# Kernel tuning notes

Measured on AMD Instinct MI355X. Metric: run time of the kernel, lower is better.

## Reference

```python
import jax, jax.numpy as jnp
import numpy as np

B, SRC_LEN, IN_DIM = 4096, 128, 16
H = 64
SEQ_LEN = 100
MEAN_DIM = 4
COV_DIM = MEAN_DIM + MEAN_DIM * (MEAN_DIM - 1) // 2  # 10
SKIP = 4


def _lin_init(key, out_d, in_d):
    k1, k2 = jax.random.split(key)
    bound = 1.0 / np.sqrt(in_d)
    W = jax.random.uniform(k1, (out_d, in_d), minval=-bound, maxval=bound, dtype=jnp.float32)
    b = jax.random.uniform(k2, (out_d,), minval=-bound, maxval=bound, dtype=jnp.float32)
    return W, b


def setup_inputs() -> dict:
    key = jax.random.key(0)
    ks = jax.random.split(key, 16)
    inp = {}
    inp["x"] = jax.random.normal(ks[0], (B, SRC_LEN, IN_DIM), dtype=jnp.float32)
    inp["trg"] = jax.random.normal(ks[1], (B, 1, SKIP), dtype=jnp.float32)
    # encoder GRU (1 layer)
    inp["enc_Wih"], inp["enc_bih"] = _lin_init(ks[2], 3 * H, IN_DIM)
    inp["enc_Whh"], inp["enc_bhh"] = _lin_init(ks[3], 3 * H, H)
    # decoder GRU (1 layer)
    inp["dec_Wih"], inp["dec_bih"] = _lin_init(ks[4], 3 * H, IN_DIM)
    inp["dec_Whh"], inp["dec_bhh"] = _lin_init(ks[5], 3 * H, H)
    # decoder.out: Linear(H -> IN_DIM)
    inp["out_W"], inp["out_b"] = _lin_init(ks[6], IN_DIM, H)
    # initEmbed: Linear(SKIP -> IN_DIM)
    inp["emb_W"], inp["emb_b"] = _lin_init(ks[7], IN_DIM, SKIP)
    # mean head: Linear(IN_DIM->H), GELU, Linear(H->MEAN_DIM)
    inp["mh_W1"], inp["mh_b1"] = _lin_init(ks[8], H, IN_DIM)
    inp["mh_W2"], inp["mh_b2"] = _lin_init(ks[9], MEAN_DIM, H)
    # cov head: Linear(IN_DIM->H), GELU, Linear(H->COV_DIM)
    inp["ch_W1"], inp["ch_b1"] = _lin_init(ks[10], H, IN_DIM)
    inp["ch_W2"], inp["ch_b2"] = _lin_init(ks[11], COV_DIM, H)
    return inp


def _gru_cell(h, xt, Wih, Whh, bih, bhh):
    # PyTorch GRU cell math. h, xt: [B, H], [B, in]
    gi = xt @ Wih.T + bih           # [B, 3H]
    gh = h @ Whh.T + bhh            # [B, 3H]
    i_r, i_z, i_n = jnp.split(gi, 3, axis=-1)
    h_r, h_z, h_n = jnp.split(gh, 3, axis=-1)
    r = jax.nn.sigmoid(i_r + h_r)
    z = jax.nn.sigmoid(i_z + h_z)
    n = jnp.tanh(i_n + r * h_n)
    return (1.0 - z) * n + z * h


def reference(x, trg, enc_Wih, enc_bih, enc_Whh, enc_bhh,
              dec_Wih, dec_bih, dec_Whh, dec_bhh,
              out_W, out_b, emb_W, emb_b,
              mh_W1, mh_b1, mh_W2, mh_b2,
              ch_W1, ch_b1, ch_W2, ch_b2):
    b = x.shape[0]
    # ---- encoder GRU over src_len; only final hidden is used downstream ----
    h0 = jnp.zeros((b, H), dtype=x.dtype)

    def enc_step(h, xt):
        h = _gru_cell(h, xt, enc_Wih, enc_Whh, enc_bih, enc_bhh)
        return h, None

    enc_h, _ = jax.lax.scan(enc_step, h0, jnp.swapaxes(x, 0, 1))

    init_in = trg[:, 0, :] @ emb_W.T + emb_b  # [B, IN_DIM]

    def dec_step(carry, _):
        h, inp = carry
        h = _gru_cell(h, inp, dec_Wih, dec_Whh, dec_bih, dec_bhh)
        o = h @ out_W.T + out_b               # [B, IN_DIM]
        nxt = jax.lax.stop_gradient(o)        # .detach() on fed-back input
        return (h, nxt), o

    (_, _), outs = jax.lax.scan(dec_step, (enc_h, init_in), None, length=SEQ_LEN)
    dec_out = jnp.swapaxes(outs, 0, 1)        # [B, SEQ_LEN, IN_DIM]

    # ---- output heads (Dropout is identity in eval) ----
    means = jax.nn.gelu(dec_out @ mh_W1.T + mh_b1, approximate=False) @ mh_W2.T + mh_b2
    covs = jax.nn.gelu(dec_out @ ch_W1.T + ch_b1, approximate=False) @ ch_W2.T + ch_b2

    inf = jnp.inf
    lower = jnp.array([-inf, -inf, -1.0, -1.0], dtype=means.dtype)
    upper = jnp.array([inf, inf, 1.0, 1.0], dtype=means.dtype)
    means = jnp.maximum(jnp.minimum(means, upper), lower)
    return means, covs
```

## Files before the change

### kernel.cpp

```cpp
#include <hip/hip_runtime.h>
#include <cstdint>
#include <cstddef>

#define BTOT    4096
#define SRCLEN  128
#define INDIM   16
#define HDIM    64
#define SEQLEN  100
#define MEANS_N (BTOT * SEQLEN * 4)

__device__ __forceinline__ float sigmoidf_(float x) {
    return __builtin_amdgcn_rcpf(1.0f + __expf(-x));
}
__device__ __forceinline__ float tanhf_(float x) {
    float e = __expf(2.0f * x);
    return 1.0f - 2.0f * __builtin_amdgcn_rcpf(e + 1.0f);
}
__device__ __forceinline__ float gelu_fast(float x) {
    float z = fabsf(x) * 0.70710678118654752440f;
    float t = __builtin_amdgcn_rcpf(1.0f + 0.3275911f * z);
    float p = t * (0.254829592f +
              t * (-0.284496736f +
              t * (1.421413741f +
              t * (-1.453152027f +
              t * 1.061405429f))));
    float er = 1.0f - p * __expf(-z * z);
    er = copysignf(er, x);
    return 0.5f * x * (1.0f + er);
}

typedef __attribute__((ext_vector_type(8))) short s8v;
typedef __attribute__((ext_vector_type(4))) float f4v;

__device__ __forceinline__ unsigned short f2bf(float x) {
    unsigned u = __float_as_uint(x);
    unsigned r = (u + 0x7FFFu + ((u >> 16) & 1u)) >> 16;
    return (unsigned short)r;
}
__device__ __forceinline__ float bf2f(unsigned short b) {
    return __uint_as_float(((unsigned)b) << 16);
}
__device__ __forceinline__ void split2(float4 a, float4 b, s8v& hi, s8v& lo) {
    float v[8] = {a.x, a.y, a.z, a.w, b.x, b.y, b.z, b.w};
    #pragma unroll
    for (int j = 0; j < 8; ++j) {
        unsigned short h = f2bf(v[j]);
        hi[j] = (short)h;
        lo[j] = (short)f2bf(v[j] - bf2f(h));
    }
}
__device__ __forceinline__ void split8(const float* v, s8v& hi, s8v& lo) {
    #pragma unroll
    for (int j = 0; j < 8; ++j) {
        unsigned short h = f2bf(v[j]);
        hi[j] = (short)h;
        lo[j] = (short)f2bf(v[j] - bf2f(h));
    }
}
__device__ __forceinline__ void load_bfrag(const float* p, s8v& hi, s8v& lo) {
    float4 a = *(const float4*)p;
    float4 b = *(const float4*)(p + 4);
    split2(a, b, hi, lo);
}

__device__ __forceinline__ float half_merge(float own_lo, float send_hi, int lane) {
    float rec = __shfl_xor(send_hi, 32, 64);
    return (lane < 32) ? own_lo : rec;
}

#define MFMA16(a, b, c) __builtin_amdgcn_mfma_f32_16x16x32_bf16((a), (b), (c), 0, 0, 0)

__global__ __launch_bounds__(256, 2) void enc_mfma_kernel(
    const float* __restrict__ x,
    const float* __restrict__ Wih, const float* __restrict__ bih,
    const float* __restrict__ Whh, const float* __restrict__ bhh,
    float* __restrict__ enc_h)
{
    const int tid  = threadIdx.x;
    const int lane = tid & 63;
    const int w    = tid >> 6;
    const int col  = lane & 15;
    const int q    = lane >> 4;
    const int u    = w * 16 + col;
    const int b0   = blockIdx.x * 8;
    const int rj0  = (q & 1) * 4 + ((q >> 1) << 1);

    __shared__ __align__(16) unsigned short hiL[2][16][72];
    __shared__ __align__(16) unsigned short loL[2][16][72];
    __shared__ __align__(16) unsigned short xhi_l[64][8][16];
    __shared__ __align__(16) unsigned short xlo_l[64][8][16];

    for (int i = tid; i < 2 * 16 * 72; i += 256) {
        ((unsigned short*)hiL)[i] = 0;
        ((unsigned short*)loL)[i] = 0;
    }

    auto stage_x = [&](int c) {
        #pragma unroll
        for (int k = 0; k < 8; ++k) {
            int f   = tid + k * 256;
            int b   = f >> 8;
            int rem = f & 255;
            int tl  = rem >> 2;
            int d4  = (rem & 3) << 2;
            const float* xp = x + ((size_t)(b0 + b) * SRCLEN + (c * 64 + tl)) * INDIM + d4;
            float4 v = *(const float4*)xp;
            float vv[4] = {v.x, v.y, v.z, v.w};
            unsigned short hh[4], ll[4];
            #pragma unroll
            for (int j = 0; j < 4; ++j) {
                hh[j] = f2bf(vv[j]);
                ll[j] = f2bf(vv[j] - bf2f(hh[j]));
            }
            *(ushort4*)&xhi_l[tl][b][d4] = make_ushort4(hh[0], hh[1], hh[2], hh[3]);
            *(ushort4*)&xlo_l[tl][b][d4] = make_ushort4(ll[0], ll[1], ll[2], ll[3]);
        }
    };

    const s8v z8 = {0, 0, 0, 0, 0, 0, 0, 0};
    const f4v z4 = {0.0f, 0.0f, 0.0f, 0.0f};

    s8v brh[3], brl[3], bzh[3], bzl[3], bnhh[2], bnhl[2], bnxh, bnxl;
    load_bfrag(Whh + (size_t)u * 64 + q * 8,              brh[0], brl[0]);
    load_bfrag(Whh + (size_t)u * 64 + 32 + q * 8,         brh[1], brl[1]);
    load_bfrag(Whh + (size_t)(64 + u) * 64 + q * 8,       bzh[0], bzl[0]);
    load_bfrag(Whh + (size_t)(64 + u) * 64 + 32 + q * 8,  bzh[1], bzl[1]);
    load_bfrag(Whh + (size_t)(128 + u) * 64 + q * 8,      bnhh[0], bnhl[0]);
    load_bfrag(Whh + (size_t)(128 + u) * 64 + 32 + q * 8, bnhh[1], bnhl[1]);
    if (q < 2) {
        load_bfrag(Wih + (size_t)u * 16 + q * 8,         brh[2], brl[2]);
        load_bfrag(Wih + (size_t)(64 + u) * 16 + q * 8,  bzh[2], bzl[2]);
        load_bfrag(Wih + (size_t)(128 + u) * 16 + q * 8, bnxh, bnxl);
    } else {
        brh[2] = z8; brl[2] = z8; bzh[2] = z8; bzl[2] = z8; bnxh = z8; bnxl = z8;
    }

    const float br   = bih[u] + bhh[u];
    const float bz   = bih[u + 64] + bhh[u + 64];
    const float bnx  = bih[u + 128];
    const float bnh  = bhh[u + 128];

    stage_x(0);
    float hold2[2] = {0.0f, 0.0f};
    __syncthreads();

    int cur = 0;
    for (int t = 0; t < SRCLEN; ++t) {
        if (t == 64) {
            stage_x(1);
            __syncthreads();
        }
        const int tl = t & 63;

        s8v xh, xl;
        if (q < 2 && col < 8) {
            xh = *(const s8v*)&xhi_l[tl][col][q * 8];
            xl = *(const s8v*)&xlo_l[tl][col][q * 8];
        } else { xh = z8; xl = z8; }

        const s8v ah0 = *(const s8v*)&hiL[cur][col][q * 8];
        const s8v al0 = *(const s8v*)&loL[cur][col][q * 8];
        const s8v ah1 = *(const s8v*)&hiL[cur][col][32 + q * 8];
        const s8v al1 = *(const s8v*)&loL[cur][col][32 + q * 8];

        f4v accr, accz, accnh, accnx;
        accr  = MFMA16(ah0, brh[0], z4);
        accz  = MFMA16(ah0, bzh[0], z4);
        accnh = MFMA16(ah0, bnhh[0], z4);
        accr  = MFMA16(ah0, brl[0], accr);
        accz  = MFMA16(ah0, bzl[0], accz);
        accnh = MFMA16(ah0, bnhl[0], accnh);
        accr  = MFMA16(al0, brh[0], accr);
        accz  = MFMA16(al0, bzh[0], accz);
        accnh = MFMA16(al0, bnhh[0], accnh);
        accr  = MFMA16(ah1, brh[1], accr);
        accz  = MFMA16(ah1, bzh[1], accz);
        accnh = MFMA16(ah1, bnhh[1], accnh);
        accr  = MFMA16(ah1, brl[1], accr);
        accz  = MFMA16(ah1, bzl[1], accz);
        accnh = MFMA16(ah1, bnhl[1], accnh);
        accr  = MFMA16(al1, brh[1], accr);
        accz  = MFMA16(al1, bzh[1], accz);
        accnh = MFMA16(al1, bnhh[1], accnh);
        accr  = MFMA16(xh, brh[2], accr);
        accz  = MFMA16(xh, bzh[2], accz);
        accnx = MFMA16(xh, bnxh, z4);
        accr  = MFMA16(xh, brl[2], accr);
        accz  = MFMA16(xh, bzl[2], accz);
        accnx = MFMA16(xh, bnxl, accnx);
        accr  = MFMA16(xl, brh[2], accr);
        accz  = MFMA16(xl, bzh[2], accz);
        accnx = MFMA16(xl, bnxh, accnx);

        float pr[2], pz[2], pnh[2], pnx[2];
        pr[0]  = half_merge(accr[0],  accr[2],  lane);
        pr[1]  = half_merge(accr[1],  accr[3],  lane);
        pz[0]  = half_merge(accz[0],  accz[2],  lane);
        pz[1]  = half_merge(accz[1],  accz[3],  lane);
        pnh[0] = half_merge(accnh[0], accnh[2], lane);
        pnh[1] = half_merge(accnh[1], accnh[3], lane);
        pnx[0] = half_merge(accnx[0], accnx[2], lane);
        pnx[1] = half_merge(accnx[1], accnx[3], lane);

        const int nxt = cur ^ 1;
        #pragma unroll
        for (int j = 0; j < 2; ++j) {
            float r  = sigmoidf_(pr[j] + br);
            float zz = sigmoidf_(pz[j] + bz);
            float n  = tanhf_(pnx[j] + bnx + r * (pnh[j] + bnh));
            float h  = (1.0f - zz) * n + zz * hold2[j];
            hold2[j] = h;
            unsigned short hh = f2bf(h);
            hiL[nxt][rj0 + j][u] = hh;
            loL[nxt][rj0 + j][u] = f2bf(h - bf2f(hh));
        }
        __syncthreads();
        cur ^= 1;
    }

    enc_h[(size_t)(b0 + rj0) * HDIM + u]     = hold2[0];
    enc_h[(size_t)(b0 + rj0 + 1) * HDIM + u] = hold2[1];
}

__global__ __launch_bounds__(256, 2) void dec_mfma_kernel(
    const float* __restrict__ trg,
    const float* __restrict__ Wih, const float* __restrict__ bih,
    const float* __restrict__ Whh, const float* __restrict__ bhh,
    const float* __restrict__ outW, const float* __restrict__ outb,
    const float* __restrict__ embW, const float* __restrict__ embb,
    const float* __restrict__ enc_h,
    float* __restrict__ dec_o)
{
    const int tid  = threadIdx.x;
    const int lane = tid & 63;
    const int w    = tid >> 6;
    const int col  = lane & 15;
    const int q    = lane >> 4;
    const int u    = w * 16 + col;
    const int b0   = blockIdx.x * 8;
    const int rj0  = (q & 1) * 4 + ((q >> 1) << 1);

    __shared__ __align__(16) unsigned short hiL[2][16][72];
    __shared__ __align__(16) unsigned short loL[2][16][72];
    __shared__ float outW_l[16][64];
    __shared__ float init_l[8][16];

    for (int i = tid; i < 16 * 64; i += 256) outW_l[i >> 6][i & 63] = outW[i];
    if (tid < 128) {
        int b = tid >> 4, jj = tid & 15;
        float s = embb[jj];
        #pragma unroll
        for (int s4 = 0; s4 < 4; ++s4)
            s = fmaf(embW[jj * 4 + s4], trg[(size_t)(b0 + b) * 4 + s4], s);
        init_l[b][jj] = s;
    }
    for (int i = tid; i < 2 * 8 * 72; i += 256) {
        int buf = i / (8 * 72);
        int rr  = (i / 72) & 7;
        int cc  = i % 72;
        hiL[buf][8 + rr][cc] = 0;
        loL[buf][8 + rr][cc] = 0;
    }
    if (tid < 128) {
        int idx = tid * 4;
        int bb = idx >> 6, uu = idx & 63;
        float4 v = *(const float4*)(enc_h + (size_t)(b0 + bb) * HDIM + uu);
        float vv[4] = {v.x, v.y, v.z, v.w};
        #pragma unroll
        for (int j = 0; j < 4; ++j) {
            unsigned short hh = f2bf(vv[j]);
            hiL[0][bb][uu + j] = hh;
            loL[0][bb][uu + j] = f2bf(vv[j] - bf2f(hh));
        }
    }
    float hold2[2];
    hold2[0] = enc_h[(size_t)(b0 + rj0) * HDIM + u];
    hold2[1] = enc_h[(size_t)(b0 + rj0 + 1) * HDIM + u];

    __syncthreads();

    const f4v z4 = {0.0f, 0.0f, 0.0f, 0.0f};

    float wh_r[16], wh_z[16], wh_n[16];
    #pragma unroll
    for (int c = 0; c < 2; ++c)
        #pragma unroll
        for (int jj = 0; jj < 8; ++jj) {
            int k = c * 32 + q * 8 + jj;
            wh_r[c * 8 + jj] = Whh[(size_t)u * 64 + k];
            wh_z[c * 8 + jj] = Whh[(size_t)(64 + u) * 64 + k];
            wh_n[c * 8 + jj] = Whh[(size_t)(128 + u) * 64 + k];
        }
    float wi_r[16], wi_z[16], wi_n[16];
    #pragma unroll
    for (int j = 0; j < 16; ++j) {
        wi_r[j] = Wih[(size_t)u * 16 + j];
        wi_z[j] = Wih[(size_t)(64 + u) * 16 + j];
        wi_n[j] = Wih[(size_t)(128 + u) * 16 + j];
    }

    float m_r[16], m_z[16], c_in[16];
    #pragma unroll
    for (int c = 0; c < 2; ++c)
        #pragma unroll
        for (int jj = 0; jj < 8; ++jj) {
            int k = c * 32 + q * 8 + jj;
            float sr = 0.0f, sz = 0.0f, sn = 0.0f;
            #pragma unroll
            for (int j = 0; j < 16; ++j) {
                float ow = outW_l[j][k];
                sr = fmaf(wi_r[j], ow, sr);
                sz = fmaf(wi_z[j], ow, sz);
                sn = fmaf(wi_n[j], ow, sn);
            }
            m_r[c * 8 + jj]  = wh_r[c * 8 + jj] + sr;
            m_z[c * 8 + jj]  = wh_z[c * 8 + jj] + sz;
            c_in[c * 8 + jj] = sn;
        }

    s8v mrh[2], mrl[2], mzh[2], mzl[2], cinh[2], cinl[2], hnh[2], hnl[2];
    split8(m_r,      mrh[0],  mrl[0]);  split8(m_r + 8,  mrh[1],  mrl[1]);
    split8(m_z,      mzh[0],  mzl[0]);  split8(m_z + 8,  mzh[1],  mzl[1]);
    split8(c_in,     cinh[0], cinl[0]); split8(c_in + 8, cinh[1], cinl[1]);
    split8(wh_n,     hnh[0],  hnl[0]);  split8(wh_n + 8, hnh[1],  hnl[1]);
    s8v r0h[2], r0l[2], z0h[2], z0l[2];
    split8(wh_r, r0h[0], r0l[0]); split8(wh_r + 8, r0h[1], r0l[1]);
    split8(wh_z, z0h[0], z0l[0]); split8(wh_z + 8, z0h[1], z0l[1]);
    s8v owh[2], owl[2];
    {
        float ov[16];
        #pragma unroll
        for (int c = 0; c < 2; ++c)
            #pragma unroll
            for (int jj = 0; jj < 8; ++jj)
                ov[c * 8 + jj] = outW_l[col][c * 32 + q * 8 + jj];
        split8(ov, owh[0], owl[0]); split8(ov + 8, owh[1], owl[1]);
    }

    float b_r = bhh[u] + bih[u];
    float b_z = bhh[u + 64] + bih[u + 64];
    float b_in = bih[u + 128];
    const float b_hn = bhh[u + 128];
    #pragma unroll
    for (int j = 0; j < 16; ++j) {
        float obj = outb[j];
        b_r  = fmaf(obj, wi_r[j], b_r);
        b_z  = fmaf(obj, wi_z[j], b_z);
        b_in = fmaf(obj, wi_n[j], b_in);
    }
    const float ob = outb[col];

    float g_r[2], g_z[2], g_n[2];
    #pragma unroll
    for (int j2 = 0; j2 < 2; ++j2) {
        int row = rj0 + j2;
        float sr = bih[u] + bhh[u];
        float sz = bih[u + 64] + bhh[u + 64];
        float sn = bih[u + 128];
        #pragma unroll
        for (int j = 0; j < 16; ++j) {
            float iv = init_l[row][j];
            sr = fmaf(wi_r[j], iv, sr);
            sz = fmaf(wi_z[j], iv, sz);
            sn = fmaf(wi_n[j], iv, sn);
        }
        g_r[j2] = sr; g_z[j2] = sz; g_n[j2] = sn;
    }

    {
        const s8v ah0 = *(const s8v*)&hiL[0][col][q * 8];
        const s8v al0 = *(const s8v*)&loL[0][col][q * 8];
        const s8v ah1 = *(const s8v*)&hiL[0][col][32 + q * 8];
        const s8v al1 = *(const s8v*)&loL[0][col][32 + q * 8];
        f4v ar, az, ahn;
        ar  = MFMA16(ah0, r0h[0], z4);
        az  = MFMA16(ah0, z0h[0], z4);
        ahn = MFMA16(ah0, hnh[0], z4);
        ar  = MFMA16(ah0, r0l[0], ar);
        az  = MFMA16(ah0, z0l[0], az);
        ahn = MFMA16(ah0, hnl[0], ahn);
        ar  = MFMA16(al0, r0h[0], ar);
        az  = MFMA16(al0, z0h[0], az);
        ahn = MFMA16(al0, hnh[0], ahn);
        ar  = MFMA16(ah1, r0h[1], ar);
        az  = MFMA16(ah1, z0h[1], az);
        ahn = MFMA16(ah1, hnh[1], ahn);
        ar  = MFMA16(ah1, r0l[1], ar);
        az  = MFMA16(ah1, z0l[1], az);
        ahn = MFMA16(ah1, hnl[1], ahn);
        ar  = MFMA16(al1, r0h[1], ar);
        az  = MFMA16(al1, z0h[1], az);
        ahn = MFMA16(al1, hnh[1], ahn);

        float pr[2], pz[2], pnh[2];
        pr[0]  = half_merge(ar[0],  ar[2],  lane);
        pr[1]  = half_merge(ar[1],  ar[3],  lane);
        pz[0]  = half_merge(az[0],  az[2],  lane);
        pz[1]  = half_merge(az[1],  az[3],  lane);
        pnh[0] = half_merge(ahn[0], ahn[2], lane);
        pnh[1] = half_merge(ahn[1], ahn[3], lane);

        #pragma unroll
        for (int j = 0; j < 2; ++j) {
            float r  = sigmoidf_(pr[j] + g_r[j]);
            float zz = sigmoidf_(pz[j] + g_z[j]);
            float n  = tanhf_(g_n[j] + r * (pnh[j] + b_hn));
            float h  = (1.0f - zz) * n + zz * hold2[j];
            hold2[j] = h;
            unsigned short hh = f2bf(h);
            hiL[1][rj0 + j][u] = hh;
            loL[1][rj0 + j][u] = f2bf(h - bf2f(hh));
        }
        __syncthreads();
    }

    for (int t = 1; t < SEQLEN; ++t) {
        const int cur = t & 1;
        const s8v ah0 = *(const s8v*)&hiL[cur][col][q * 8];
        const s8v al0 = *(const s8v*)&loL[cur][col][q * 8];
        const s8v ah1 = *(const s8v*)&hiL[cur][col][32 + q * 8];
        const s8v al1 = *(const s8v*)&loL[cur][col][32 + q * 8];

        if (w == 0) {
            f4v oa;
            oa = MFMA16(ah0, owh[0], z4);
            oa = MFMA16(ah0, owl[0], oa);
            oa = MFMA16(al0, owh[0], oa);
            oa = MFMA16(ah1, owh[1], oa);
            oa = MFMA16(ah1, owl[1], oa);
            oa = MFMA16(al1, owh[1], oa);
            if (q < 2) {
                #pragma unroll
                for (int i = 0; i < 4; ++i)
                    dec_o[(((size_t)(b0 + q * 4 + i) * SEQLEN) + (t - 1)) * INDIM + col] = oa[i] + ob;
            }
        }

        f4v ar, az, ain, ahn;
        ar  = MFMA16(ah0, mrh[0], z4);
        az  = MFMA16(ah0, mzh[0], z4);
        ain = MFMA16(ah0, cinh[0], z4);
        ahn = MFMA16(ah0, hnh[0], z4);
        ar  = MFMA16(ah0, mrl[0], ar);
        az  = MFMA16(ah0, mzl[0], az);
        ain = MFMA16(ah0, cinl[0], ain);
        ahn = MFMA16(ah0, hnl[0], ahn);
        ar  = MFMA16(al0, mrh[0], ar);
        az  = MFMA16(al0, mzh[0], az);
        ain = MFMA16(al0, cinh[0], ain);
        ahn = MFMA16(al0, hnh[0], ahn);
        ar  = MFMA16(ah1, mrh[1], ar);
        az  = MFMA16(ah1, mzh[1], az);
        ain = MFMA16(ah1, cinh[1], ain);
        ahn = MFMA16(ah1, hnh[1], ahn);
        ar  = MFMA16(ah1, mrl[1], ar);
        az  = MFMA16(ah1, mzl[1], az);
        ain = MFMA16(ah1, cinl[1], ain);
        ahn = MFMA16(ah1, hnl[1], ahn);
        ar  = MFMA16(al1, mrh[1], ar);
        az  = MFMA16(al1, mzh[1], az);
        ain = MFMA16(al1, cinh[1], ain);
        ahn = MFMA16(al1, hnh[1], ahn);

        float pr[2], pz[2], pin[2], pnh[2];
        pr[0]  = half_merge(ar[0],  ar[2],  lane);
        pr[1]  = half_merge(ar[1],  ar[3],  lane);
        pz[0]  = half_merge(az[0],  az[2],  lane);
        pz[1]  = half_merge(az[1],  az[3],  lane);
        pin[0] = half_merge(ain[0], ain[2], lane);
        pin[1] = half_merge(ain[1], ain[3], lane);
        pnh[0] = half_merge(ahn[0], ahn[2], lane);
        pnh[1] = half_merge(ahn[1], ahn[3], lane);

        const int nxt = cur ^ 1;
        #pragma unroll
        for (int j = 0; j < 2; ++j) {
            float r  = sigmoidf_(pr[j] + b_r);
            float zz = sigmoidf_(pz[j] + b_z);
            float n  = tanhf_(pin[j] + b_in + r * (pnh[j] + b_hn));
            float h  = (1.0f - zz) * n + zz * hold2[j];
            hold2[j] = h;
            unsigned short hh = f2bf(h);
            hiL[nxt][rj0 + j][u] = hh;
            loL[nxt][rj0 + j][u] = f2bf(h - bf2f(hh));
        }
        __syncthreads();
    }

    if (w == 0) {
        const s8v ah0 = *(const s8v*)&hiL[0][col][q * 8];
        const s8v al0 = *(const s8v*)&loL[0][col][q * 8];
        const s8v ah1 = *(const s8v*)&hiL[0][col][32 + q * 8];
        const s8v al1 = *(const s8v*)&loL[0][col][32 + q * 8];
        f4v oa;
        oa = MFMA16(ah0, owh[0], z4);
        oa = MFMA16(ah0, owl[0], oa);
        oa = MFMA16(al0, owh[0], oa);
        oa = MFMA16(ah1, owh[1], oa);
        oa = MFMA16(ah1, owl[1], oa);
        oa = MFMA16(al1, owh[1], oa);
        if (q < 2) {
            #pragma unroll
            for (int i = 0; i < 4; ++i)
                dec_o[(((size_t)(b0 + q * 4 + i) * SEQLEN) + (SEQLEN - 1)) * INDIM + col] = oa[i] + ob;
        }
    }
}

__global__ void heads_kernel(
    const float* __restrict__ dec_o,
    const float* __restrict__ mW1, const float* __restrict__ mb1,
    const float* __restrict__ mW2, const float* __restrict__ mb2,
    const float* __restrict__ cW1, const float* __restrict__ cb1,
    const float* __restrict__ cW2, const float* __restrict__ cb2,
    float* __restrict__ out)
{
    const size_t r = (size_t)blockIdx.x * 256 + threadIdx.x;

    float o16[16];
    {
        const float4* op = (const float4*)(dec_o + r * 16);
        #pragma unroll
        for (int c = 0; c < 4; ++c) {
            float4 v = op[c];
            o16[4 * c + 0] = v.x; o16[4 * c + 1] = v.y;
            o16[4 * c + 2] = v.z; o16[4 * c + 3] = v.w;
        }
    }

    float m[4], cv[10];
    #pragma unroll
    for (int j = 0; j < 4; ++j)  m[j]  = mb2[j];
    #pragma unroll
    for (int j = 0; j < 10; ++j) cv[j] = cb2[j];

    #pragma unroll 8
    for (int hu = 0; hu < 64; ++hu) {
        const float* w1m = mW1 + hu * 16;
        float hm = mb1[hu];
        #pragma unroll
        for (int i = 0; i < 16; ++i) hm = fmaf(w1m[i], o16[i], hm);
        float gm = gelu_fast(hm);
        #pragma unroll
        for (int j = 0; j < 4; ++j) m[j] = fmaf(mW2[j * 64 + hu], gm, m[j]);

        const float* w1c = cW1 + hu * 16;
        float hc = cb1[hu];
        #pragma unroll
        for (int i = 0; i < 16; ++i) hc = fmaf(w1c[i], o16[i], hc);
        float gc = gelu_fast(hc);
        #pragma unroll
        for (int j = 0; j < 10; ++j) cv[j] = fmaf(cW2[j * 64 + hu], gc, cv[j]);
    }

    m[2] = fminf(fmaxf(m[2], -1.0f), 1.0f);
    m[3] = fminf(fmaxf(m[3], -1.0f), 1.0f);

    float* means = out;
    float* covs  = out + MEANS_N;
    #pragma unroll
    for (int j = 0; j < 4; ++j)  means[r * 4 + j]  = m[j];
    #pragma unroll
    for (int j = 0; j < 10; ++j) covs[r * 10 + j]  = cv[j];
}

extern "C" void kernel_launch(void* const* d_in, const int* in_sizes, int n_in,
                              void* d_out, int out_size, void* d_ws, size_t ws_size,
                              hipStream_t stream)
{
    const float* x    = (const float*)d_in[0];
    const float* trg  = (const float*)d_in[1];
    const float* eWih = (const float*)d_in[2];
    const float* ebih = (const float*)d_in[3];
    const float* eWhh = (const float*)d_in[4];
    const float* ebhh = (const float*)d_in[5];
    const float* dWih = (const float*)d_in[6];
    const float* dbih = (const float*)d_in[7];
    const float* dWhh = (const float*)d_in[8];
    const float* dbhh = (const float*)d_in[9];
    const float* outW = (const float*)d_in[10];
    const float* outb = (const float*)d_in[11];
    const float* embW = (const float*)d_in[12];
    const float* embb = (const float*)d_in[13];
    const float* mW1  = (const float*)d_in[14];
    const float* mb1  = (const float*)d_in[15];
    const float* mW2  = (const float*)d_in[16];
    const float* mb2  = (const float*)d_in[17];
    const float* cW1  = (const float*)d_in[18];
    const float* cb1  = (const float*)d_in[19];
    const float* cW2  = (const float*)d_in[20];
    const float* cb2  = (const float*)d_in[21];

    float* ws    = (float*)d_ws;
    float* enc_h = ws;
    float* dec_o = ws + (size_t)BTOT * HDIM;
    float* outp  = (float*)d_out;

    enc_mfma_kernel<<<dim3(BTOT / 8), dim3(256), 0, stream>>>(x, eWih, ebih, eWhh, ebhh, enc_h);
    dec_mfma_kernel<<<dim3(BTOT / 8), dim3(256), 0, stream>>>(trg, dWih, dbih, dWhh, dbhh,
                                                              outW, outb, embW, embb, enc_h, dec_o);
    heads_kernel<<<dim3((BTOT * SEQLEN) / 256), dim3(256), 0, stream>>>(
        dec_o, mW1, mb1, mW2, mb2, cW1, cb1, cW2, cb2, outp);
}
```

Measured before the change: 388.3 us.

## Use permlane32_swap merges, branchless x loads, rotated output wave, LDS-staged head weights

Replaces the shfl_xor-based half merge with the permlane32_swap builtin, which avoids an LDS-routed shuffle on the critical recurrent path. Adds a zero-padded row to the staged x buffers so the per-step x fragment loads become unconditional. Rotates which wave computes the decoder output projection each step instead of always wave 0, spreading that load across waves. Stages the head weights into shared memory as float4-readable rows to replace scalar global loads. The permlane32_swap builtin depends on gfx950 support, and the extra LDS use raises shared-memory footprint.

```diff
diff --git a/kernel.cpp b/kernel.cpp
--- a/kernel.cpp
+++ b/kernel.cpp
@@ -63,9 +63,12 @@
     split2(a, b, hi, lo);
 }
 
-__device__ __forceinline__ float half_merge(float own_lo, float send_hi, int lane) {
-    float rec = __shfl_xor(send_hi, 32, 64);
-    return (lane < 32) ? own_lo : rec;
+typedef __attribute__((ext_vector_type(2))) unsigned int u2v;
+__device__ __forceinline__ float half_merge(float own_lo, float send_hi) {
+    u2v r = __builtin_amdgcn_permlane32_swap(__float_as_uint(own_lo),
+                                             __float_as_uint(send_hi),
+                                             false, false);
+    return __uint_as_float(r[0]);
 }
 
 #define MFMA16(a, b, c) __builtin_amdgcn_mfma_f32_16x16x32_bf16((a), (b), (c), 0, 0, 0)
@@ -87,12 +90,16 @@
 
     __shared__ __align__(16) unsigned short hiL[2][16][72];
     __shared__ __align__(16) unsigned short loL[2][16][72];
-    __shared__ __align__(16) unsigned short xhi_l[64][8][16];
-    __shared__ __align__(16) unsigned short xlo_l[64][8][16];
+    __shared__ __align__(16) unsigned short xhi_l[64][9][16];
+    __shared__ __align__(16) unsigned short xlo_l[64][9][16];
 
     for (int i = tid; i < 2 * 16 * 72; i += 256) {
         ((unsigned short*)hiL)[i] = 0;
         ((unsigned short*)loL)[i] = 0;
+    }
+    for (int i = tid; i < 64 * 16; i += 256) {
+        xhi_l[i >> 4][8][i & 15] = 0;
+        xlo_l[i >> 4][8][i & 15] = 0;
     }
 
     auto stage_x = [&](int c) {
@@ -140,6 +147,11 @@
     const float bnx  = bih[u + 128];
     const float bnh  = bhh[u + 128];
 
+    const int xb   = (q < 2) ? (col & 7) : 8;
+    const int xoff = (q & 1) * 8;
+    const unsigned short* xh_base = &xhi_l[0][xb][xoff];
+    const unsigned short* xl_base = &xlo_l[0][xb][xoff];
+
     stage_x(0);
     float hold2[2] = {0.0f, 0.0f};
     __syncthreads();
@@ -152,11 +164,8 @@
         }
         const int tl = t & 63;
 
-        s8v xh, xl;
-        if (q < 2 && col < 8) {
-            xh = *(const s8v*)&xhi_l[tl][col][q * 8];
-            xl = *(const s8v*)&xlo_l[tl][col][q * 8];
-        } else { xh = z8; xl = z8; }
+        const s8v xh = *(const s8v*)(xh_base + (size_t)tl * 144);
+        const s8v xl = *(const s8v*)(xl_base + (size_t)tl * 144);
 
         const s8v ah0 = *(const s8v*)&hiL[cur][col][q * 8];
         const s8v al0 = *(const s8v*)&loL[cur][col][q * 8];
@@ -193,14 +202,14 @@
         accnx = MFMA16(xl, bnxh, accnx);
 
         float pr[2], pz[2], pnh[2], pnx[2];
-        pr[0]  = half_merge(accr[0],  accr[2],  lane);
-        pr[1]  = half_merge(accr[1],  accr[3],  lane);
-        pz[0]  = half_merge(accz[0],  accz[2],  lane);
-        pz[1]  = half_merge(accz[1],  accz[3],  lane);
-        pnh[0] = half_merge(accnh[0], accnh[2], lane);
-        pnh[1] = half_merge(accnh[1], accnh[3], lane);
-        pnx[0] = half_merge(accnx[0], accnx[2], lane);
-        pnx[1] = half_merge(accnx[1], accnx[3], lane);
+        pr[0]  = half_merge(accr[0],  accr[2]);
+        pr[1]  = half_merge(accr[1],  accr[3]);
+        pz[0]  = half_merge(accz[0],  accz[2]);
+        pz[1]  = half_merge(accz[1],  accz[3]);
+        pnh[0] = half_merge(accnh[0], accnh[2]);
+        pnh[1] = half_merge(accnh[1], accnh[3]);
+        pnx[0] = half_merge(accnx[0], accnx[2]);
+        pnx[1] = half_merge(accnx[1], accnx[3]);
 
         const int nxt = cur ^ 1;
         #pragma unroll
@@ -393,12 +402,12 @@
         ahn = MFMA16(al1, hnh[1], ahn);
 
         float pr[2], pz[2], pnh[2];
-        pr[0]  = half_merge(ar[0],  ar[2],  lane);
-        pr[1]  = half_merge(ar[1],  ar[3],  lane);
-        pz[0]  = half_merge(az[0],  az[2],  lane);
-        pz[1]  = half_merge(az[1],  az[3],  lane);
-        pnh[0] = half_merge(ahn[0], ahn[2], lane);
-        pnh[1] = half_merge(ahn[1], ahn[3], lane);
+        pr[0]  = half_merge(ar[0],  ar[2]);
+        pr[1]  = half_merge(ar[1],  ar[3]);
+        pz[0]  = half_merge(az[0],  az[2]);
+        pz[1]  = half_merge(az[1],  az[3]);
+        pnh[0] = half_merge(ahn[0], ahn[2]);
+        pnh[1] = half_merge(ahn[1], ahn[3]);
 
         #pragma unroll
         for (int j = 0; j < 2; ++j) {
@@ -421,7 +430,7 @@
         const s8v ah1 = *(const s8v*)&hiL[cur][col][32 + q * 8];
         const s8v al1 = *(const s8v*)&loL[cur][col][32 + q * 8];
 
-        if (w == 0) {
+        if (w == ((t - 1) & 3)) {
             f4v oa;
             oa = MFMA16(ah0, owh[0], z4);
             oa = MFMA16(ah0, owl[0], oa);
@@ -463,14 +472,14 @@
         ahn = MFMA16(al1, hnh[1], ahn);
 
         float pr[2], pz[2], pin[2], pnh[2];
-        pr[0]  = half_merge(ar[0],  ar[2],  lane);
-        pr[1]  = half_merge(ar[1],  ar[3],  lane);
-        pz[0]  = half_merge(az[0],  az[2],  lane);
-        pz[1]  = half_merge(az[1],  az[3],  lane);
-        pin[0] = half_merge(ain[0], ain[2], lane);
-        pin[1] = half_merge(ain[1], ain[3], lane);
-        pnh[0] = half_merge(ahn[0], ahn[2], lane);
-        pnh[1] = half_merge(ahn[1], ahn[3], lane);
+        pr[0]  = half_merge(ar[0],  ar[2]);
+        pr[1]  = half_merge(ar[1],  ar[3]);
+        pz[0]  = half_merge(az[0],  az[2]);
+        pz[1]  = half_merge(az[1],  az[3]);
+        pin[0] = half_merge(ain[0], ain[2]);
+        pin[1] = half_merge(ain[1], ain[3]);
+        pnh[0] = half_merge(ahn[0], ahn[2]);
+        pnh[1] = half_merge(ahn[1], ahn[3]);
 
         const int nxt = cur ^ 1;
         #pragma unroll
@@ -507,7 +516,7 @@
     }
 }
 
-__global__ void heads_kernel(
+__global__ __launch_bounds__(256) void heads_kernel(
     const float* __restrict__ dec_o,
     const float* __restrict__ mW1, const float* __restrict__ mb1,
     const float* __restrict__ mW2, const float* __restrict__ mb2,
@@ -515,7 +524,27 @@
     const float* __restrict__ cW2, const float* __restrict__ cb2,
     float* __restrict__ out)
 {
-    const size_t r = (size_t)blockIdx.x * 256 + threadIdx.x;
+    const int tid = threadIdx.x;
+
+    __shared__ __align__(16) float lW1m[64][16];
+    __shared__ __align__(16) float lW1c[64][16];
+    __shared__ __align__(16) float lW2t[64][16];
+
+    for (int i = tid; i < 1024; i += 256) {
+        lW1m[i >> 4][i & 15] = mW1[i];
+        lW1c[i >> 4][i & 15] = cW1[i];
+    }
+    if (tid < 64) {
+        #pragma unroll
+        for (int j = 0; j < 4; ++j)  lW2t[tid][j]     = mW2[j * 64 + tid];
+        #pragma unroll
+        for (int j = 0; j < 10; ++j) lW2t[tid][4 + j] = cW2[j * 64 + tid];
+        lW2t[tid][14] = mb1[tid];
+        lW2t[tid][15] = cb1[tid];
+    }
+    __syncthreads();
+
+    const size_t r = (size_t)blockIdx.x * 256 + tid;
 
     float o16[16];
     {
@@ -534,23 +563,49 @@
     #pragma unroll
     for (int j = 0; j < 10; ++j) cv[j] = cb2[j];
 
-    #pragma unroll 8
+    #pragma unroll 4
     for (int hu = 0; hu < 64; ++hu) {
-        const float* w1m = mW1 + hu * 16;
-        float hm = mb1[hu];
-        #pragma unroll
-        for (int i = 0; i < 16; ++i) hm = fmaf(w1m[i], o16[i], hm);
+        const float4 a0 = *(const float4*)&lW1m[hu][0];
+        const float4 a1 = *(const float4*)&lW1m[hu][4];
+        const float4 a2 = *(const float4*)&lW1m[hu][8];
+        const float4 a3 = *(const float4*)&lW1m[hu][12];
+        const float4 c0 = *(const float4*)&lW1c[hu][0];
+        const float4 c1 = *(const float4*)&lW1c[hu][4];
+        const float4 c2 = *(const float4*)&lW1c[hu][8];
+        const float4 c3 = *(const float4*)&lW1c[hu][12];
+        const float4 t0 = *(const float4*)&lW2t[hu][0];
+        const float4 t1 = *(const float4*)&lW2t[hu][4];
+        const float4 t2 = *(const float4*)&lW2t[hu][8];
+        const float4 t3 = *(const float4*)&lW2t[hu][12];
+
+        float hm = t3.z;
+        hm = fmaf(a0.x, o16[0],  hm); hm = fmaf(a0.y, o16[1],  hm);
+        hm = fmaf(a0.z, o16[2],  hm); hm = fmaf(a0.w, o16[3],  hm);
+        hm = fmaf(a1.x, o16[4],  hm); hm = fmaf(a1.y, o16[5],  hm);
+        hm = fmaf(a1.z, o16[6],  hm); hm = fmaf(a1.w, o16[7],  hm);
+        hm = fmaf(a2.x, o16[8],  hm); hm = fmaf(a2.y, o16[9],  hm);
+        hm = fmaf(a2.z, o16[10], hm); hm = fmaf(a2.w, o16[11], hm);
+        hm = fmaf(a3.x, o16[12], hm); hm = fmaf(a3.y, o16[13], hm);
+        hm = fmaf(a3.z, o16[14], hm); hm = fmaf(a3.w, o16[15], hm);
         float gm = gelu_fast(hm);
-        #pragma unroll
-        for (int j = 0; j < 4; ++j) m[j] = fmaf(mW2[j * 64 + hu], gm, m[j]);
-
-        const float* w1c = cW1 + hu * 16;
-        float hc = cb1[hu];
-        #pragma unroll
-        for (int i = 0; i < 16; ++i) hc = fmaf(w1c[i], o16[i], hc);
+        m[0] = fmaf(t0.x, gm, m[0]); m[1] = fmaf(t0.y, gm, m[1]);
+        m[2] = fmaf(t0.z, gm, m[2]); m[3] = fmaf(t0.w, gm, m[3]);
+
+        float hc = t3.w;
+        hc = fmaf(c0.x, o16[0],  hc); hc = fmaf(c0.y, o16[1],  hc);
+        hc = fmaf(c0.z, o16[2],  hc); hc = fmaf(c0.w, o16[3],  hc);
+        hc = fmaf(c1.x, o16[4],  hc); hc = fmaf(c1.y, o16[5],  hc);
+        hc = fmaf(c1.z, o16[6],  hc); hc = fmaf(c1.w, o16[7],  hc);
+        hc = fmaf(c2.x, o16[8],  hc); hc = fmaf(c2.y, o16[9],  hc);
+        hc = fmaf(c2.z, o16[10], hc); hc = fmaf(c2.w, o16[11], hc);
+        hc = fmaf(c3.x, o16[12], hc); hc = fmaf(c3.y, o16[13], hc);
+        hc = fmaf(c3.z, o16[14], hc); hc = fmaf(c3.w, o16[15], hc);
         float gc = gelu_fast(hc);
-        #pragma unroll
-        for (int j = 0; j < 10; ++j) cv[j] = fmaf(cW2[j * 64 + hu], gc, cv[j]);
+        cv[0] = fmaf(t1.x, gc, cv[0]); cv[1] = fmaf(t1.y, gc, cv[1]);
+        cv[2] = fmaf(t1.z, gc, cv[2]); cv[3] = fmaf(t1.w, gc, cv[3]);
+        cv[4] = fmaf(t2.x, gc, cv[4]); cv[5] = fmaf(t2.y, gc, cv[5]);
+        cv[6] = fmaf(t2.z, gc, cv[6]); cv[7] = fmaf(t2.w, gc, cv[7]);
+        cv[8] = fmaf(t3.x, gc, cv[8]); cv[9] = fmaf(t3.y, gc, cv[9]);
     }
 
     m[2] = fminf(fmaxf(m[2], -1.0f), 1.0f);
```

Result: faster. 347.9 us (-10.4%).
